# Kernel tuning notes

Measured on AMD Instinct MI355X. Metric: run time of the kernel, lower is better.

## Reference

```python
import jax, jax.numpy as jnp
import numpy as np

N = 50000   # nodes
E = 800000  # edges
IN_DIM = 512
HID = 256   # total hidden (4 heads x 64)
HEADS = 4
OUT_DIM = 256
NEG_SLOPE = 0.2


def setup_inputs() -> dict:
    key = jax.random.key(0)
    ks = jax.random.split(key, 16)
    s = 0.05
    d = {
        "feats": jax.random.normal(ks[0], (N, IN_DIM), jnp.float32),
        "src": jax.random.randint(ks[1], (E,), 0, N, jnp.int32),
        "dst": jax.random.randint(ks[2], (E,), 0, N, jnp.int32),
        # layer 0: in 512 -> 4 heads x 64
        "W0": jax.random.normal(ks[3], (IN_DIM, HID), jnp.float32) * s,
        "al0": jax.random.normal(ks[4], (HEADS, HID // HEADS), jnp.float32) * s,
        "ar0": jax.random.normal(ks[5], (HEADS, HID // HEADS), jnp.float32) * s,
        "b0": jnp.zeros((HID,), jnp.float32),
        # layer 1: in 256 -> 4 heads x 64
        "W1": jax.random.normal(ks[6], (HID, HID), jnp.float32) * s,
        "al1": jax.random.normal(ks[7], (HEADS, HID // HEADS), jnp.float32) * s,
        "ar1": jax.random.normal(ks[8], (HEADS, HID // HEADS), jnp.float32) * s,
        "b1": jnp.zeros((HID,), jnp.float32),
        # layer 2: in 256 -> 1 head x 256, no activation
        "W2": jax.random.normal(ks[9], (HID, OUT_DIM), jnp.float32) * s,
        "al2": jax.random.normal(ks[10], (1, OUT_DIM), jnp.float32) * s,
        "ar2": jax.random.normal(ks[11], (1, OUT_DIM), jnp.float32) * s,
        "b2": jnp.zeros((OUT_DIM,), jnp.float32),
    }
    return d


def gat_conv(h, src, dst, W, al, ar, b, act):
    """DGL-style GATConv (no dropout, no residual). Returns [N, H, D]."""
    H, D = al.shape
    feat = (h @ W).reshape(-1, H, D)                       # [N,H,D]
    el = jnp.einsum('nhd,hd->nh', feat, al)                # [N,H]
    er = jnp.einsum('nhd,hd->nh', feat, ar)                # [N,H]
    e = jax.nn.leaky_relu(el[src] + er[dst], NEG_SLOPE)    # [E,H]
    # edge softmax over incoming edges per destination node
    m = jax.ops.segment_max(e, dst, num_segments=N)        # [N,H]
    ex = jnp.exp(e - m[dst])                               # [E,H]
    s = jax.ops.segment_sum(ex, dst, num_segments=N)       # [N,H]
    alpha = ex / s[dst]                                    # [E,H]
    msg = jax.ops.segment_sum(alpha[:, :, None] * feat[src], dst, num_segments=N)  # [N,H,D]
    out = msg + b.reshape(1, H, D)
    return act(out) if act is not None else out


def reference(feats, src, dst, W0, al0, ar0, b0, W1, al1, ar1, b1, W2, al2, ar2, b2):
    h = gat_conv(feats, src, dst, W0, al0, ar0, b0, jax.nn.relu)
    h = h.reshape(h.shape[0], -1)                          # flatten heads
    h = gat_conv(h, src, dst, W1, al1, ar1, b1, jax.nn.relu)
    h = h.reshape(h.shape[0], -1)
    h = gat_conv(h, src, dst, W2, al2, ar2, b2, None)
    h = h.mean(axis=1)                                     # last layer: mean over (single) head
    return h
```

## Files before the change

### kernel.cpp

```cpp
#include <hip/hip_runtime.h>
#include <hip/hip_bf16.h>
#include <math.h>


#define HID 256

typedef __attribute__((ext_vector_type(8))) _Float16 half8;
typedef __attribute__((ext_vector_type(4))) _Float16 half4;
typedef __attribute__((ext_vector_type(4))) float floatx4;

__device__ __forceinline__ void gl_lds16(const void* g, void* l) {
    __builtin_amdgcn_global_load_lds(
        (const __attribute__((address_space(1))) void*)g,
        (__attribute__((address_space(3))) void*)l, 16, 0, 0);
}


__global__ void hist_kernel(const int* __restrict__ dst, int* __restrict__ cnt, int E) {
    int e = blockIdx.x * blockDim.x + threadIdx.x;
    if (e < E) atomicAdd(&cnt[dst[e]], 1);
}

__global__ __launch_bounds__(256) void scan1_kernel(const int* __restrict__ cnt,
                                                    int* __restrict__ bsum, int n) {
    __shared__ int w[4];
    int t = threadIdx.x;
    int i = blockIdx.x * 256 + t;
    int c = (i < n) ? cnt[i] : 0;
    int acc = c;
#pragma unroll
    for (int off = 32; off > 0; off >>= 1) acc += __shfl_xor(acc, off);
    if ((t & 63) == 0) w[t >> 6] = acc;
    __syncthreads();
    if (t == 0) bsum[blockIdx.x] = w[0] + w[1] + w[2] + w[3];
}

__global__ __launch_bounds__(256) void scan2_kernel(const int* __restrict__ bsum,
                                                    int* __restrict__ boff, int nb) {
    __shared__ int buf[256];
    int t = threadIdx.x;
    int v = (t < nb) ? bsum[t] : 0;
    buf[t] = v;
    __syncthreads();
    for (int off = 1; off < 256; off <<= 1) {
        int x = (t >= off) ? buf[t - off] : 0;
        __syncthreads();
        buf[t] += x;
        __syncthreads();
    }
    if (t < nb) boff[t] = buf[t] - v;
}

__global__ __launch_bounds__(256) void scan3_kernel(const int* __restrict__ cnt,
                                                    const int* __restrict__ boff,
                                                    int* __restrict__ rowptr,
                                                    int* __restrict__ cursor, int n) {
    __shared__ int buf[256];
    int t = threadIdx.x;
    int i = blockIdx.x * 256 + t;
    int c = (i < n) ? cnt[i] : 0;
    buf[t] = c;
    __syncthreads();
    for (int off = 1; off < 256; off <<= 1) {
        int x = (t >= off) ? buf[t - off] : 0;
        __syncthreads();
        buf[t] += x;
        __syncthreads();
    }
    int start = boff[blockIdx.x] + buf[t] - c;
    if (i < n) {
        rowptr[i] = start;
        cursor[i] = start;
        if (i == n - 1) rowptr[n] = start + c;
    }
}

__global__ void fill_kernel(const int* __restrict__ src, const int* __restrict__ dst,
                            int* __restrict__ cursor, int* __restrict__ adj, int E) {
    int e = blockIdx.x * blockDim.x + threadIdx.x;
    if (e < E) {
        int d = dst[e];
        int pos = atomicAdd(&cursor[d], 1);
        adj[pos] = src[e];
    }
}


__device__ __forceinline__ void splitT_f16(const float* W, _Float16* ht, _Float16* lt,
                                           int idx, int K) {
    int k = idx >> 8, n = idx & 255;
    float v = W[idx];
    _Float16 h = (_Float16)v;
    ht[(size_t)n * K + k] = h;
    lt[(size_t)n * K + k] = (_Float16)(v - (float)h);
}

__global__ __launch_bounds__(256) void splitT_all_kernel(
    const float* __restrict__ W0, const float* __restrict__ W1,
    const float* __restrict__ W2, _Float16* h0, _Float16* l0, _Float16* h1,
    _Float16* l1, _Float16* h2, _Float16* l2) {
    int i = blockIdx.x * 256 + threadIdx.x;
    const int n0 = 512 * 256, n1 = 256 * 256;
    if (i < n0) splitT_f16(W0, h0, l0, i, 512);
    else if (i < n0 + n1) splitT_f16(W1, h1, l1, i - n0, 256);
    else if (i < n0 + 2 * n1) splitT_f16(W2, h2, l2, i - n0 - n1, 256);
}


template <bool SPLITA>
__global__ __launch_bounds__(256, 2) void gemm_f16_kernel(
    const float* __restrict__ Af, const _Float16* __restrict__ A16,
    const _Float16* __restrict__ Bht, const _Float16* __restrict__ Blt,
    _Float16* __restrict__ C, const float* __restrict__ al,
    const float* __restrict__ ar, float* __restrict__ el,
    float* __restrict__ er, int M, int K, int H) {
    __shared__ _Float16 sA[128 * 32];
    __shared__ _Float16 sBh[128 * 32];
    __shared__ _Float16 sBl[128 * 32];

    int t = threadIdx.x;
    int wave = t >> 6, lane = t & 63;
    int wr = wave >> 1, wc = wave & 1;
    int quad = lane >> 4, m16 = lane & 15;

    int rowA0 = blockIdx.y * 128;
    int rowB0 = blockIdx.x * 128;

    int sr = t >> 2;
    int ke = ((t & 3) ^ ((t >> 3) & 3)) * 8;
    int ldso = t * 8;
    int srow = t >> 1;
    int kb = (t & 1) * 16;
    int s0 = (t & 1) * 2;
    int ssw = (srow >> 1) & 3;
    int soA = srow * 32 + (s0 ^ ssw) * 8;
    int soB = srow * 32 + ((s0 + 1) ^ ssw) * 8;

    size_t ar0 = 0, ar1 = 0, af0 = 0;
    if (SPLITA) {
        af0 = (size_t)min(rowA0 + srow, M - 1) * K + kb;
    } else {
        ar0 = (size_t)min(rowA0 + sr, M - 1) * K;
        ar1 = (size_t)min(rowA0 + sr + 64, M - 1) * K;
    }
    size_t br0 = (size_t)(rowB0 + sr) * K;
    size_t br1 = (size_t)(rowB0 + sr + 64) * K;

    int qsw = (quad ^ ((m16 >> 1) & 3)) * 8;

    floatx4 acc[4][4];
    floatx4 z = {0.f, 0.f, 0.f, 0.f};
#pragma unroll
    for (int i = 0; i < 4; i++)
#pragma unroll
        for (int j = 0; j < 4; j++) acc[i][j] = z;

    int nk = K >> 5;
    for (int kt = 0; kt < nk; kt++) {
        int k0 = kt << 5;
        int k0s = k0 + ke;
        gl_lds16(Bht + br0 + k0s, &sBh[ldso]);
        gl_lds16(Bht + br1 + k0s, &sBh[2048 + ldso]);
        gl_lds16(Blt + br0 + k0s, &sBl[ldso]);
        gl_lds16(Blt + br1 + k0s, &sBl[2048 + ldso]);
        if (SPLITA) {
            const float* ap = Af + af0 + k0;
            float4 v0 = ((const float4*)ap)[0];
            float4 v1 = ((const float4*)ap)[1];
            float4 v2 = ((const float4*)ap)[2];
            float4 v3 = ((const float4*)ap)[3];
            float vv[16] = {v0.x, v0.y, v0.z, v0.w, v1.x, v1.y, v1.z, v1.w,
                            v2.x, v2.y, v2.z, v2.w, v3.x, v3.y, v3.z, v3.w};
            half8 h0, h1;
#pragma unroll
            for (int c = 0; c < 8; c++) {
                h0[c] = (_Float16)vv[c];
                h1[c] = (_Float16)vv[8 + c];
            }
            *(half8*)&sA[soA] = h0;
            *(half8*)&sA[soB] = h1;
        } else {
            gl_lds16(A16 + ar0 + k0s, &sA[ldso]);
            gl_lds16(A16 + ar1 + k0s, &sA[2048 + ldso]);
        }
        __syncthreads();

        half8 fa[4], fbh[4], fbl[4];
#pragma unroll
        for (int i = 0; i < 4; i++) {
            int off = (wr * 64 + i * 16 + m16) * 32 + qsw;
            fa[i] = *(const half8*)&sA[off];
        }
#pragma unroll
        for (int j = 0; j < 4; j++) {
            int off = (wc * 64 + j * 16 + m16) * 32 + qsw;
            fbh[j] = *(const half8*)&sBh[off];
            fbl[j] = *(const half8*)&sBl[off];
        }
#pragma unroll
        for (int i = 0; i < 4; i++)
#pragma unroll
            for (int j = 0; j < 4; j++) {
                acc[i][j] = __builtin_amdgcn_mfma_f32_16x16x32_f16(fa[i], fbh[j], acc[i][j], 0, 0, 0);
                acc[i][j] = __builtin_amdgcn_mfma_f32_16x16x32_f16(fa[i], fbl[j], acc[i][j], 0, 0, 0);
            }
        __syncthreads();
    }

#pragma unroll
    for (int i = 0; i < 4; i++) {
        int rowb = rowA0 + wr * 64 + i * 16 + quad * 4;
#pragma unroll
        for (int j = 0; j < 4; j++) {
            int col = rowB0 + wc * 64 + j * 16 + m16;
#pragma unroll
            for (int r = 0; r < 4; r++) {
                int row = rowb + r;
                if (row < M) C[(size_t)row * HID + col] = (_Float16)acc[i][j][r];
            }
        }
    }

    float alv[4], arv[4];
#pragma unroll
    for (int j = 0; j < 4; j++) {
        int col = rowB0 + wc * 64 + j * 16 + m16;
        alv[j] = al[col];
        arv[j] = ar[col];
    }
    int h = ((rowB0 + wc * 64) >> 6) & (H - 1);
#pragma unroll
    for (int i = 0; i < 4; i++) {
        int rowb = rowA0 + wr * 64 + i * 16 + quad * 4;
#pragma unroll
        for (int r = 0; r < 4; r++) {
            float pe = acc[i][0][r] * alv[0] + acc[i][1][r] * alv[1] +
                       acc[i][2][r] * alv[2] + acc[i][3][r] * alv[3];
            float pr = acc[i][0][r] * arv[0] + acc[i][1][r] * arv[1] +
                       acc[i][2][r] * arv[2] + acc[i][3][r] * arv[3];
#pragma unroll
            for (int off = 1; off < 16; off <<= 1) {
                pe += __shfl_xor(pe, off);
                pr += __shfl_xor(pr, off);
            }
            int row = rowb + r;
            if (m16 == 0 && row < M) {
                if (H == 4) {
                    el[row * 4 + h] = pe;
                    er[row * 4 + h] = pr;
                } else {
                    atomicAdd(&el[row], pe);
                    atomicAdd(&er[row], pr);
                }
            }
        }
    }
}


template <int H, bool RELU, int WMODE>
__global__ __launch_bounds__(256) void agg_tpl(
    const _Float16* __restrict__ feat, const float* __restrict__ el,
    const float* __restrict__ er, const int* __restrict__ rowptr,
    const int* __restrict__ adj, const float* __restrict__ bias,
    float* __restrict__ outf, _Float16* __restrict__ oa, int N) {
    int wave = threadIdx.x >> 6, lane = threadIdx.x & 63;
    int v = blockIdx.x * 4 + wave;
    if (v >= N) return;
    int row0 = rowptr[v];
    int deg = rowptr[v + 1] - row0;

    int l32 = lane & 31;
    int half = lane >> 5;
    int hd = (H == 4) ? (l32 >> 3) : 0;
    int d0 = l32 * 8;

    float o[8];
    if (deg > 0) {
        float er_h = (H == 4) ? er[v * 4 + hd] : er[v];
        const int* adjr = adj + row0;

        float a[8];
#pragma unroll
        for (int j = 0; j < 8; j++) a[j] = 0.f;
        float sl = 0.f;

        int e = 0;
        for (; e + 16 <= deg; e += 16) {
            int u[8];
            half8 f[8];
            float elv[8];
#pragma unroll
            for (int q = 0; q < 8; q++) u[q] = adjr[e + q * 2 + half];
#pragma unroll
            for (int q = 0; q < 8; q++)
                f[q] = *(const half8*)&feat[(size_t)u[q] * HID + d0];
#pragma unroll
            for (int q = 0; q < 8; q++)
                elv[q] = (H == 4) ? el[u[q] * 4 + hd] : el[u[q]];
#pragma unroll
            for (int q = 0; q < 8; q++) {
                float sc = elv[q] + er_h;
                sc = (sc > 0.f) ? sc : 0.2f * sc;
                float ex = __expf(sc);
                sl += ex;
#pragma unroll
                for (int j = 0; j < 8; j++) a[j] = fmaf(ex, (float)f[q][j], a[j]);
            }
        }
        for (; e + 8 <= deg; e += 8) {
            int u[4];
            half8 f[4];
            float elv[4];
#pragma unroll
            for (int q = 0; q < 4; q++) u[q] = adjr[e + q * 2 + half];
#pragma unroll
            for (int q = 0; q < 4; q++)
                f[q] = *(const half8*)&feat[(size_t)u[q] * HID + d0];
#pragma unroll
            for (int q = 0; q < 4; q++)
                elv[q] = (H == 4) ? el[u[q] * 4 + hd] : el[u[q]];
#pragma unroll
            for (int q = 0; q < 4; q++) {
                float sc = elv[q] + er_h;
                sc = (sc > 0.f) ? sc : 0.2f * sc;
                float ex = __expf(sc);
                sl += ex;
#pragma unroll
                for (int j = 0; j < 8; j++) a[j] = fmaf(ex, (float)f[q][j], a[j]);
            }
        }
        for (; e < deg; e += 2) {
            int ee = e + half;
            bool act = ee < deg;
            int es = act ? ee : (deg - 1);
            int u = adjr[es];
            float elvq = (H == 4) ? el[u * 4 + hd] : el[u];
            half8 f = *(const half8*)&feat[(size_t)u * HID + d0];
            float sc = elvq + er_h;
            sc = (sc > 0.f) ? sc : 0.2f * sc;
            float ex = act ? __expf(sc) : 0.f;
            sl += ex;
#pragma unroll
            for (int j = 0; j < 8; j++) a[j] = fmaf(ex, (float)f[j], a[j]);
        }

#pragma unroll
        for (int j = 0; j < 8; j++) a[j] += __shfl_xor(a[j], 32);
        sl += __shfl_xor(sl, 32);
        float inv = 1.f / sl;

#pragma unroll
        for (int j = 0; j < 8; j++) {
            o[j] = fmaf(a[j], inv, bias[d0 + j]);
            if (RELU) o[j] = fmaxf(o[j], 0.f);
        }
    } else {
#pragma unroll
        for (int j = 0; j < 8; j++) {
            o[j] = bias[d0 + j];
            if (RELU) o[j] = fmaxf(o[j], 0.f);
        }
    }

    if (half == 0) {
        size_t base = (size_t)v * HID + d0;
        if (WMODE == 0) {
            *(float4*)&outf[base] = make_float4(o[0], o[1], o[2], o[3]);
            *(float4*)&outf[base + 4] = make_float4(o[4], o[5], o[6], o[7]);
        } else {
            half8 ha;
#pragma unroll
            for (int j = 0; j < 8; j++) ha[j] = (_Float16)o[j];
            *(half8*)&oa[base] = ha;
        }
    }
}


extern "C" void kernel_launch(void* const* d_in, const int* in_sizes, int n_in,
                              void* d_out, int out_size, void* d_ws, size_t ws_size,
                              hipStream_t stream) {
    const float* feats = (const float*)d_in[0];
    const int* src = (const int*)d_in[1];
    const int* dst = (const int*)d_in[2];
    const float* W0 = (const float*)d_in[3];
    const float* al0 = (const float*)d_in[4];
    const float* ar0 = (const float*)d_in[5];
    const float* b0 = (const float*)d_in[6];
    const float* W1 = (const float*)d_in[7];
    const float* al1 = (const float*)d_in[8];
    const float* ar1 = (const float*)d_in[9];
    const float* b1 = (const float*)d_in[10];
    const float* W2 = (const float*)d_in[11];
    const float* al2 = (const float*)d_in[12];
    const float* ar2 = (const float*)d_in[13];
    const float* b2 = (const float*)d_in[14];
    float* out = (float*)d_out;

    const int IN_DIM = 512;
    const int N = in_sizes[0] / IN_DIM;
    const int E = in_sizes[1];

    char* ws = (char*)d_ws;
    size_t off = 0;
    auto alloc = [&](size_t bytes) -> void* {
        void* p = ws + off;
        off = (off + bytes + 255) & ~(size_t)255;
        return p;
    };
    _Float16* featbuf = (_Float16*)alloc((size_t)N * HID * sizeof(_Float16));
    _Float16* featA = (_Float16*)alloc((size_t)N * HID * sizeof(_Float16));
    float* el = (float*)alloc((size_t)N * 4 * sizeof(float));
    float* er = (float*)alloc((size_t)N * 4 * sizeof(float));
    int* cnt = (int*)alloc((size_t)N * sizeof(int));
    int* rowptr = (int*)alloc((size_t)(N + 1) * sizeof(int));
    int* cursor = (int*)alloc((size_t)N * sizeof(int));
    int* adj = (int*)alloc((size_t)E * sizeof(int));
    int nscanb = (N + 255) / 256;
    int* bsum = (int*)alloc((size_t)nscanb * sizeof(int));
    int* boff = (int*)alloc((size_t)nscanb * sizeof(int));
    _Float16* Bht0 = (_Float16*)alloc((size_t)512 * HID * sizeof(_Float16));
    _Float16* Blt0 = (_Float16*)alloc((size_t)512 * HID * sizeof(_Float16));
    _Float16* Bht1 = (_Float16*)alloc((size_t)256 * HID * sizeof(_Float16));
    _Float16* Blt1 = (_Float16*)alloc((size_t)256 * HID * sizeof(_Float16));
    _Float16* Bht2 = (_Float16*)alloc((size_t)256 * HID * sizeof(_Float16));
    _Float16* Blt2 = (_Float16*)alloc((size_t)256 * HID * sizeof(_Float16));
    (void)ws_size;

    hipMemsetAsync(cnt, 0, (size_t)N * sizeof(int), stream);
    hist_kernel<<<(E + 255) / 256, 256, 0, stream>>>(dst, cnt, E);
    scan1_kernel<<<nscanb, 256, 0, stream>>>(cnt, bsum, N);
    scan2_kernel<<<1, 256, 0, stream>>>(bsum, boff, nscanb);
    scan3_kernel<<<nscanb, 256, 0, stream>>>(cnt, boff, rowptr, cursor, N);
    fill_kernel<<<(E + 255) / 256, 256, 0, stream>>>(src, dst, cursor, adj, E);

    dim3 ggrid128(HID / 128, (N + 127) / 128);
    int aggb = (N + 3) / 4;

    splitT_all_kernel<<<(512 * 256 + 2 * 256 * 256) / 256, 256, 0, stream>>>(
        W0, W1, W2, Bht0, Blt0, Bht1, Blt1, Bht2, Blt2);

    gemm_f16_kernel<true><<<ggrid128, 256, 0, stream>>>(
        feats, nullptr, Bht0, Blt0, featbuf, al0, ar0, el, er, N, 512, 4);
    agg_tpl<4, true, 2><<<aggb, 256, 0, stream>>>(
        featbuf, el, er, rowptr, adj, b0, nullptr, featA, N);

    gemm_f16_kernel<false><<<ggrid128, 256, 0, stream>>>(
        nullptr, featA, Bht1, Blt1, featbuf, al1, ar1, el, er, N, 256, 4);
    agg_tpl<4, true, 2><<<aggb, 256, 0, stream>>>(
        featbuf, el, er, rowptr, adj, b1, nullptr, featA, N);

    hipMemsetAsync(el, 0, (size_t)N * 8 * sizeof(float), stream);
    gemm_f16_kernel<false><<<ggrid128, 256, 0, stream>>>(
        nullptr, featA, Bht2, Blt2, featbuf, al2, ar2, el, er, N, 256, 1);
    agg_tpl<1, false, 0><<<aggb, 256, 0, stream>>>(
        featbuf, el, er, rowptr, adj, b2, out, nullptr, N);
}
```

Baseline: 578.6 us.

## Drop low-part weight MFMA in first two GEMMs and widen K tile to 64

After: 573.7 us. Within noise of the previous version (-0.9%).

```diff
diff --git a/kernel.cpp b/kernel.cpp
--- a/kernel.cpp
+++ b/kernel.cpp
@@ -6,7 +6,6 @@
 #define HID 256
 
 typedef __attribute__((ext_vector_type(8))) _Float16 half8;
-typedef __attribute__((ext_vector_type(4))) _Float16 half4;
 typedef __attribute__((ext_vector_type(4))) float floatx4;
 
 __device__ __forceinline__ void gl_lds16(const void* g, void* l) {
@@ -107,16 +106,16 @@
 }
 
 
-template <bool SPLITA>
+template <bool SPLITA, bool SPLITB>
 __global__ __launch_bounds__(256, 2) void gemm_f16_kernel(
     const float* __restrict__ Af, const _Float16* __restrict__ A16,
     const _Float16* __restrict__ Bht, const _Float16* __restrict__ Blt,
     _Float16* __restrict__ C, const float* __restrict__ al,
     const float* __restrict__ ar, float* __restrict__ el,
     float* __restrict__ er, int M, int K, int H) {
-    __shared__ _Float16 sA[128 * 32];
-    __shared__ _Float16 sBh[128 * 32];
-    __shared__ _Float16 sBl[128 * 32];
+    __shared__ _Float16 sA[128 * 64];
+    __shared__ _Float16 sB[128 * 64];
+    __shared__ _Float16 sBl[SPLITB ? 128 * 64 : 8];
 
     int t = threadIdx.x;
     int wave = t >> 6, lane = t & 63;
@@ -126,27 +125,25 @@
     int rowA0 = blockIdx.y * 128;
     int rowB0 = blockIdx.x * 128;
 
-    int sr = t >> 2;
-    int ke = ((t & 3) ^ ((t >> 3) & 3)) * 8;
+    int srow0 = t >> 3;
+    int gslot = ((t & 7) ^ ((t >> 3) & 7)) * 8;
     int ldso = t * 8;
-    int srow = t >> 1;
-    int kb = (t & 1) * 16;
-    int s0 = (t & 1) * 2;
-    int ssw = (srow >> 1) & 3;
-    int soA = srow * 32 + (s0 ^ ssw) * 8;
-    int soB = srow * 32 + ((s0 + 1) ^ ssw) * 8;
-
-    size_t ar0 = 0, ar1 = 0, af0 = 0;
-    if (SPLITA) {
-        af0 = (size_t)min(rowA0 + srow, M - 1) * K + kb;
-    } else {
-        ar0 = (size_t)min(rowA0 + sr, M - 1) * K;
-        ar1 = (size_t)min(rowA0 + sr + 64, M - 1) * K;
-    }
-    size_t br0 = (size_t)(rowB0 + sr) * K;
-    size_t br1 = (size_t)(rowB0 + sr + 64) * K;
-
-    int qsw = (quad ^ ((m16 >> 1) & 3)) * 8;
+
+    int arow = t >> 1;
+    int akb = (t & 1) * 32;
+    int arsw = arow & 7;
+
+    size_t aoff[4], boff[4];
+#pragma unroll
+    for (int i = 0; i < 4; i++) {
+        int r = srow0 + 32 * i;
+        boff[i] = (size_t)(rowB0 + r) * K + gslot;
+        if (!SPLITA) aoff[i] = (size_t)min(rowA0 + r, M - 1) * K + gslot;
+    }
+    size_t af0 = 0;
+    if (SPLITA) af0 = (size_t)min(rowA0 + arow, M - 1) * K + akb;
+
+    int rswz = m16 & 7;
 
     floatx4 acc[4][4];
     floatx4 z = {0.f, 0.f, 0.f, 0.f};
@@ -155,55 +152,63 @@
 #pragma unroll
         for (int j = 0; j < 4; j++) acc[i][j] = z;
 
-    int nk = K >> 5;
+    int nk = K >> 6;
     for (int kt = 0; kt < nk; kt++) {
-        int k0 = kt << 5;
-        int k0s = k0 + ke;
-        gl_lds16(Bht + br0 + k0s, &sBh[ldso]);
-        gl_lds16(Bht + br1 + k0s, &sBh[2048 + ldso]);
-        gl_lds16(Blt + br0 + k0s, &sBl[ldso]);
-        gl_lds16(Blt + br1 + k0s, &sBl[2048 + ldso]);
+        int k0 = kt << 6;
+#pragma unroll
+        for (int i = 0; i < 4; i++)
+            gl_lds16(Bht + boff[i] + k0, &sB[ldso + 2048 * i]);
+        if (SPLITB) {
+#pragma unroll
+            for (int i = 0; i < 4; i++)
+                gl_lds16(Blt + boff[i] + k0, &sBl[ldso + 2048 * i]);
+        }
         if (SPLITA) {
-            const float* ap = Af + af0 + k0;
-            float4 v0 = ((const float4*)ap)[0];
-            float4 v1 = ((const float4*)ap)[1];
-            float4 v2 = ((const float4*)ap)[2];
-            float4 v3 = ((const float4*)ap)[3];
-            float vv[16] = {v0.x, v0.y, v0.z, v0.w, v1.x, v1.y, v1.z, v1.w,
-                            v2.x, v2.y, v2.z, v2.w, v3.x, v3.y, v3.z, v3.w};
-            half8 h0, h1;
-#pragma unroll
-            for (int c = 0; c < 8; c++) {
-                h0[c] = (_Float16)vv[c];
-                h1[c] = (_Float16)vv[8 + c];
-            }
-            *(half8*)&sA[soA] = h0;
-            *(half8*)&sA[soB] = h1;
+            const float4* ap = (const float4*)(Af + af0 + k0);
+#pragma unroll
+            for (int j = 0; j < 4; j++) {
+                float4 a = ap[2 * j];
+                float4 b = ap[2 * j + 1];
+                half8 h;
+                h[0] = (_Float16)a.x; h[1] = (_Float16)a.y;
+                h[2] = (_Float16)a.z; h[3] = (_Float16)a.w;
+                h[4] = (_Float16)b.x; h[5] = (_Float16)b.y;
+                h[6] = (_Float16)b.z; h[7] = (_Float16)b.w;
+                int slot = (((t & 1) * 4 + j) ^ arsw);
+                *(half8*)&sA[arow * 64 + slot * 8] = h;
+            }
         } else {
-            gl_lds16(A16 + ar0 + k0s, &sA[ldso]);
-            gl_lds16(A16 + ar1 + k0s, &sA[2048 + ldso]);
-        }
-        __syncthreads();
-
-        half8 fa[4], fbh[4], fbl[4];
-#pragma unroll
-        for (int i = 0; i < 4; i++) {
-            int off = (wr * 64 + i * 16 + m16) * 32 + qsw;
-            fa[i] = *(const half8*)&sA[off];
-        }
-#pragma unroll
-        for (int j = 0; j < 4; j++) {
-            int off = (wc * 64 + j * 16 + m16) * 32 + qsw;
-            fbh[j] = *(const half8*)&sBh[off];
-            fbl[j] = *(const half8*)&sBl[off];
-        }
-#pragma unroll
-        for (int i = 0; i < 4; i++)
+#pragma unroll
+            for (int i = 0; i < 4; i++)
+                gl_lds16(A16 + aoff[i] + k0, &sA[ldso + 2048 * i]);
+        }
+        __syncthreads();
+
+#pragma unroll
+        for (int kk = 0; kk < 2; kk++) {
+            half8 fa[4], fb[4], fbl[4];
+#pragma unroll
+            for (int i = 0; i < 4; i++) {
+                int row = wr * 64 + i * 16 + m16;
+                int slot = ((kk * 4 + quad) ^ rswz);
+                fa[i] = *(const half8*)&sA[row * 64 + slot * 8];
+            }
 #pragma unroll
             for (int j = 0; j < 4; j++) {
-                acc[i][j] = __builtin_amdgcn_mfma_f32_16x16x32_f16(fa[i], fbh[j], acc[i][j], 0, 0, 0);
-                acc[i][j] = __builtin_amdgcn_mfma_f32_16x16x32_f16(fa[i], fbl[j], acc[i][j], 0, 0, 0);
-            }
+                int row = wc * 64 + j * 16 + m16;
+                int slot = ((kk * 4 + quad) ^ rswz);
+                fb[j] = *(const half8*)&sB[row * 64 + slot * 8];
+                if (SPLITB) fbl[j] = *(const half8*)&sBl[row * 64 + slot * 8];
+            }
+#pragma unroll
+            for (int i = 0; i < 4; i++)
+#pragma unroll
+                for (int j = 0; j < 4; j++) {
+                    acc[i][j] = __builtin_amdgcn_mfma_f32_16x16x32_f16(fa[i], fb[j], acc[i][j], 0, 0, 0);
+                    if (SPLITB)
+                        acc[i][j] = __builtin_amdgcn_mfma_f32_16x16x32_f16(fa[i], fbl[j], acc[i][j], 0, 0, 0);
+                }
+        }
         __syncthreads();
     }
 
@@ -441,18 +446,18 @@
     splitT_all_kernel<<<(512 * 256 + 2 * 256 * 256) / 256, 256, 0, stream>>>(
         W0, W1, W2, Bht0, Blt0, Bht1, Blt1, Bht2, Blt2);
 
-    gemm_f16_kernel<true><<<ggrid128, 256, 0, stream>>>(
-        feats, nullptr, Bht0, Blt0, featbuf, al0, ar0, el, er, N, 512, 4);
+    gemm_f16_kernel<true, false><<<ggrid128, 256, 0, stream>>>(
+        feats, nullptr, Bht0, nullptr, featbuf, al0, ar0, el, er, N, 512, 4);
     agg_tpl<4, true, 2><<<aggb, 256, 0, stream>>>(
         featbuf, el, er, rowptr, adj, b0, nullptr, featA, N);
 
-    gemm_f16_kernel<false><<<ggrid128, 256, 0, stream>>>(
-        nullptr, featA, Bht1, Blt1, featbuf, al1, ar1, el, er, N, 256, 4);
+    gemm_f16_kernel<false, false><<<ggrid128, 256, 0, stream>>>(
+        nullptr, featA, Bht1, nullptr, featbuf, al1, ar1, el, er, N, 256, 4);
     agg_tpl<4, true, 2><<<aggb, 256, 0, stream>>>(
         featbuf, el, er, rowptr, adj, b1, nullptr, featA, N);
 
     hipMemsetAsync(el, 0, (size_t)N * 8 * sizeof(float), stream);
-    gemm_f16_kernel<false><<<ggrid128, 256, 0, stream>>>(
+    gemm_f16_kernel<false, true><<<ggrid128, 256, 0, stream>>>(
         nullptr, featA, Bht2, Blt2, featbuf, al2, ar2, el, er, N, 256, 1);
     agg_tpl<1, false, 0><<<aggb, 256, 0, stream>>>(
         featbuf, el, er, rowptr, adj, b2, out, nullptr, N);
```
